# Optimization experiments

Hardware: AMD Instinct MI355X
Metric: run time of the kernel (lower is better)

Reference implementation:

```python
import jax, jax.numpy as jnp
import numpy as np

N = 50000
E = 800000
IN_DIM = 16
H = 128
L = 4
EDGE_DIM = 7
LN_EPS = 1e-5


def _linear_params(key, fan_in, fan_out):
    kw, kb = jax.random.split(key)
    w = jax.random.normal(kw, (fan_in, fan_out), jnp.float32) * 0.02
    b = jax.random.normal(kb, (fan_out,), jnp.float32) * 0.02
    return w, b


def setup_inputs() -> dict:
    key = jax.random.key(0)
    ks = jax.random.split(key, 20)
    x = jax.random.normal(ks[0], (N, IN_DIM), jnp.float32)
    pos = jax.random.uniform(ks[1], (N, 3), jnp.float32) * 10.0
    row = jax.random.randint(ks[2], (E,), 0, N, jnp.int32)
    # guarantee no self-loops so distance > 0 (radius_graph uses loop=False)
    off = jax.random.randint(ks[3], (E,), 1, N, jnp.int32)
    col = (row + off) % N
    edge_index = jnp.stack([row, col], axis=0)

    W_in, b_in = _linear_params(ks[4], IN_DIM, H)

    def stack_layers(kbase, fan_in, fan_out):
        ws, bs = [], []
        for l in range(L):
            w, b = _linear_params(jax.random.fold_in(kbase, l), fan_in, fan_out)
            ws.append(w); bs.append(b)
        return jnp.stack(ws), jnp.stack(bs)

    We1, be1 = stack_layers(ks[5], 2 * H + EDGE_DIM, H)
    We2, be2 = stack_layers(ks[6], H, H)
    We3, be3 = stack_layers(ks[7], H, H)
    Wn1, bn1 = stack_layers(ks[8], H + H, H)
    Wn2, bn2 = stack_layers(ks[9], H, H)
    Wn3, bn3 = stack_layers(ks[10], H, H)
    ln_g = jnp.ones((L, H), jnp.float32)
    ln_b = jnp.zeros((L, H), jnp.float32)

    return {
        'x': x, 'pos': pos, 'edge_index': edge_index,
        'W_in': W_in, 'b_in': b_in,
        'We1': We1, 'be1': be1, 'We2': We2, 'be2': be2, 'We3': We3, 'be3': be3,
        'Wn1': Wn1, 'bn1': bn1, 'Wn2': Wn2, 'bn2': bn2, 'Wn3': Wn3, 'bn3': bn3,
        'ln_g': ln_g, 'ln_b': ln_b,
    }


def reference(x, pos, edge_index, W_in, b_in, We1, be1, We2, be2, We3, be3,
              Wn1, bn1, Wn2, bn2, Wn3, bn3, ln_g, ln_b):
    n = x.shape[0]
    row, col = edge_index[0], edge_index[1]  # row=source, col=target (PyG)
    rel_pos = pos[col] - pos[row]                       # (E, 3)
    dist = jnp.linalg.norm(rel_pos, axis=1, keepdims=True)  # (E, 1)
    edge_attr = jnp.concatenate([rel_pos, dist], axis=1)    # (E, 4)

    h = x @ W_in + b_in  # (N, H)
    num_layers = We1.shape[0]
    for l in range(num_layers):
        mom = h[:, 3:6]
        rel_mom = mom[col] - mom[row]                        # (E, 3)
        ea = jnp.concatenate([edge_attr, rel_mom], axis=1)   # (E, 7)
        # PyG: x_i = x[target=col], x_j = x[source=row]; EdgeMLP concats [h_i, h_j, ea]
        m = jnp.concatenate([h[col], h[row], ea], axis=1)    # (E, 2H+7)
        m = jax.nn.relu(m @ We1[l] + be1[l])
        m = jax.nn.relu(m @ We2[l] + be2[l])
        m = m @ We3[l] + be3[l]                              # (E, H)
        agg = jax.ops.segment_sum(m, col, num_segments=n)    # scatter-add to targets
        u = jnp.concatenate([h, agg], axis=1)                # (N, 2H)
        u = jax.nn.relu(u @ Wn1[l] + bn1[l])
        u = jax.nn.relu(u @ Wn2[l] + bn2[l])
        u = u @ Wn3[l] + bn3[l]                              # (N, H)
        h = h + u
        mean = jnp.mean(h, axis=-1, keepdims=True)
        var = jnp.mean(jnp.square(h - mean), axis=-1, keepdims=True)
        h = (h - mean) * jax.lax.rsqrt(var + LN_EPS) * ln_g[l] + ln_b[l]
    return h
```

## Files before the change

kernel.cpp:

```cpp
#include <hip/hip_runtime.h>
#include <stdint.h>

#define NN 50000
#define NE 800000
#define HD 128
#define NL 4
#define NM 64
#define EB 128

typedef __bf16 bf16x8 __attribute__((ext_vector_type(8)));
typedef __bf16 bf16x4 __attribute__((ext_vector_type(4)));
typedef float  f32x4  __attribute__((ext_vector_type(4)));

__device__ __forceinline__ f32x4 mfma16(bf16x8 a, bf16x8 b, f32x4 c) {
  return __builtin_amdgcn_mfma_f32_16x16x32_bf16(a, b, c, 0, 0, 0);
}

template<int MT, int NT>
__device__ __forceinline__ void zero_acc(f32x4 (&acc)[MT][NT]) {
#pragma unroll
  for (int i = 0; i < MT; ++i)
#pragma unroll
    for (int j = 0; j < NT; ++j) acc[i][j] = f32x4{0.f, 0.f, 0.f, 0.f};
}

template<int MT, int NT, int KS>
__device__ __forceinline__ void gemm_chunk(const __bf16* A, int sa,
    const __bf16* __restrict__ Bt, int Krow, int k0,
    int m_off, int n_off, int lane, f32x4 (&acc)[MT][NT])
{
  const int arow = lane & 15;
  const int quad = lane >> 4;
  bf16x8 b[KS][NT];
#pragma unroll
  for (int ks = 0; ks < KS; ++ks)
#pragma unroll
    for (int nt = 0; nt < NT; ++nt)
      b[ks][nt] = *reinterpret_cast<const bf16x8*>(
          Bt + (size_t)(n_off + nt * 16 + arow) * Krow + k0 + ks * 32 + quad * 8);
#pragma unroll
  for (int ks = 0; ks < KS; ++ks) {
    const int k = k0 + ks * 32 + quad * 8;
    bf16x8 a[MT];
#pragma unroll
    for (int mt = 0; mt < MT; ++mt)
      a[mt] = *reinterpret_cast<const bf16x8*>(A + (m_off + mt * 16 + arow) * sa + k);
#pragma unroll
    for (int mt = 0; mt < MT; ++mt)
#pragma unroll
      for (int nt = 0; nt < NT; ++nt)
        acc[mt][nt] = mfma16(a[mt], b[ks][nt], acc[mt][nt]);
  }
}

template<int MT, int NT, bool RELU>
__device__ __forceinline__ void store_tile(__bf16* O, int so,
    const float* __restrict__ bias, int m_off, int n_off, int lane,
    f32x4 (&acc)[MT][NT])
{
  const int quad = lane >> 4;
  const int cl = lane & 15;
#pragma unroll
  for (int nt = 0; nt < NT; ++nt) {
    const int col = n_off + nt * 16 + cl;
    const float bv = bias[col];
#pragma unroll
    for (int mt = 0; mt < MT; ++mt)
#pragma unroll
      for (int r = 0; r < 4; ++r) {
        const int row = m_off + mt * 16 + quad * 4 + r;
        float v = acc[mt][nt][r] + bv;
        if (RELU) v = fmaxf(v, 0.f);
        O[row * so + col] = (__bf16)v;
      }
  }
}

__global__ void prep_w(const float* __restrict__ W, __bf16* __restrict__ Wt,
                       int K0, int Kp) {
  int idx = blockIdx.x * 256 + threadIdx.x;
  int total = NL * HD * Kp;
  if (idx >= total) return;
  int l = idx / (HD * Kp);
  int rem = idx - l * HD * Kp;
  int n = rem / Kp;
  int k = rem - n * Kp;
  float v = (k < K0) ? W[((size_t)l * K0 + k) * HD + n] : 0.f;
  Wt[idx] = (__bf16)v;
}

__global__ void prep_pqw(const float* __restrict__ We1,
                         __bf16* __restrict__ Wtopt, __bf16* __restrict__ Wbott) {
  int idx = blockIdx.x * 256 + threadIdx.x;
  if (idx >= NL * HD * HD) return;
  int l = idx / (HD * HD);
  int rem = idx - l * HD * HD;
  int n = rem >> 7;
  int k = rem & 127;
  const float* W = We1 + (size_t)l * 263 * HD;
  float extra = (k >= 3 && k < 6) ? W[(260 + k - 3) * HD + n] : 0.f;
  Wtopt[idx] = (__bf16)(W[k * HD + n] + extra);
  Wbott[idx] = (__bf16)(W[(128 + k) * HD + n] - extra);
}

__global__ void h0_kernel(const float* __restrict__ x, const float* __restrict__ W,
                          const float* __restrict__ b, float* __restrict__ H32,
                          __bf16* __restrict__ HB) {
  int idx = blockIdx.x * 256 + threadIdx.x;
  if (idx >= NN * HD) return;
  int node = idx >> 7, j = idx & 127;
  const float* xr = x + node * 16;
  float s = b[j];
#pragma unroll
  for (int k = 0; k < 16; ++k) s += xr[k] * W[k * HD + j];
  H32[idx] = s;
  HB[idx] = (__bf16)s;
}

__global__ void hist_kernel(const int* __restrict__ ei, int* __restrict__ cnt) {
  int e = blockIdx.x * 256 + threadIdx.x;
  if (e < NE) atomicAdd(&cnt[ei[NE + e]], 1);
}

__global__ void scan_kernel(const int* __restrict__ cnt, int* __restrict__ cur) {
  __shared__ int wsum[16];
  __shared__ int carry;
  int t = threadIdx.x;
  int lane = t & 63, wid = t >> 6;
  if (t == 0) carry = 0;
  __syncthreads();
  for (int base = 0; base < NN; base += 1024) {
    int v = (base + t < NN) ? cnt[base + t] : 0;
    int incl = v;
#pragma unroll
    for (int off = 1; off < 64; off <<= 1) {
      int u = __shfl_up(incl, off, 64);
      if (lane >= off) incl += u;
    }
    if (lane == 63) wsum[wid] = incl;
    __syncthreads();
    int woff = 0;
    for (int k = 0; k < wid; ++k) woff += wsum[k];
    int c = carry;
    if (base + t < NN) cur[base + t] = c + woff + incl - v;
    __syncthreads();
    if (t == 1023) carry = c + woff + incl;
    __syncthreads();
  }
}

__global__ void scatter_kernel(const int* __restrict__ ei, int* __restrict__ cur,
                               int* __restrict__ ROWS, int* __restrict__ COLS) {
  int e = blockIdx.x * 256 + threadIdx.x;
  if (e < NE) {
    int r = ei[e], c = ei[NE + e];
    int p = atomicAdd(&cur[c], 1);
    ROWS[p] = r;
    COLS[p] = c;
  }
}

__global__ void dist_kernel(const float* __restrict__ pos,
                            const int* __restrict__ ROWS, const int* __restrict__ COLS,
                            __bf16* __restrict__ DSTb) {
  int p = blockIdx.x * 256 + threadIdx.x;
  if (p >= NE) return;
  int r = ROWS[p], c = COLS[p];
  float dx = pos[c * 3 + 0] - pos[r * 3 + 0];
  float dy = pos[c * 3 + 1] - pos[r * 3 + 1];
  float dz = pos[c * 3 + 2] - pos[r * 3 + 2];
  DSTb[p] = (__bf16)sqrtf(dx * dx + dy * dy + dz * dz);
}

__global__ __launch_bounds__(256, 4) void pq_kernel(
    const __bf16* __restrict__ HB, const float* __restrict__ pos,
    const __bf16* __restrict__ Wtopt, const __bf16* __restrict__ Wbott,
    const float* __restrict__ W4xyz,
    const float* __restrict__ be1,
    __bf16* __restrict__ PB, __bf16* __restrict__ QB)
{
  const int task = blockIdx.x * 4 + (threadIdx.x >> 6);
  const int lane = threadIdx.x & 63;
  const int g = task & 1;
  const int base = (task >> 1) * 32;
  if (base >= NN) return;
  const int arow = lane & 15, quad = lane >> 4, cl = lane & 15;

  const __bf16* Wt = g ? Wbott : Wtopt;
  __bf16* O = g ? QB : PB;
  f32x4 acc[2][8];
  zero_acc(acc);
#pragma unroll
  for (int ks = 0; ks < 4; ++ks) {
    const int k = ks * 32 + quad * 8;
    bf16x8 b[8];
#pragma unroll
    for (int nt = 0; nt < 8; ++nt)
      b[nt] = *reinterpret_cast<const bf16x8*>(Wt + (size_t)(nt * 16 + arow) * HD + k);
    bf16x8 a[2];
#pragma unroll
    for (int mt = 0; mt < 2; ++mt) {
      int row = base + mt * 16 + arow;
      if (row >= NN) row = NN - 1;
      a[mt] = *reinterpret_cast<const bf16x8*>(HB + (size_t)row * HD + k);
    }
#pragma unroll
    for (int mt = 0; mt < 2; ++mt)
#pragma unroll
      for (int nt = 0; nt < 8; ++nt)
        acc[mt][nt] = mfma16(a[mt], b[nt], acc[mt][nt]);
  }
  float px[2][4], py[2][4], pz[2][4];
#pragma unroll
  for (int mt = 0; mt < 2; ++mt)
#pragma unroll
    for (int r = 0; r < 4; ++r) {
      int row = base + mt * 16 + quad * 4 + r;
      if (row >= NN) row = NN - 1;
      px[mt][r] = pos[row * 3 + 0];
      py[mt][r] = pos[row * 3 + 1];
      pz[mt][r] = pos[row * 3 + 2];
    }
#pragma unroll
  for (int nt = 0; nt < 8; ++nt) {
    const int col = nt * 16 + cl;
    const float w0 = W4xyz[col], w1 = W4xyz[HD + col], w2 = W4xyz[2 * HD + col];
    const float bb = g ? 0.f : be1[col];
#pragma unroll
    for (int mt = 0; mt < 2; ++mt)
#pragma unroll
      for (int r = 0; r < 4; ++r) {
        const int row = base + mt * 16 + quad * 4 + r;
        if (row < NN) {
          float dot = px[mt][r] * w0 + py[mt][r] * w1 + pz[mt][r] * w2;
          float v = acc[mt][nt][r] + (g ? -dot : dot) + bb;
          O[(size_t)row * HD + col] = (__bf16)v;
        }
      }
  }
}

__global__ __launch_bounds__(512, 4) void edge_kernel(
    const __bf16* __restrict__ PB, const __bf16* __restrict__ QB,
    const __bf16* __restrict__ DSTb,
    const int* __restrict__ ROWS, const int* __restrict__ COLS,
    const float* __restrict__ w4d,
    const __bf16* __restrict__ We2t, const __bf16* __restrict__ We3t,
    const float* __restrict__ be2, const float* __restrict__ be3,
    float* __restrict__ AGG)
{
  __shared__ __bf16 S1[EB * 136];
  __shared__ __bf16 S2[EB * 136];
  __shared__ float w4ds[HD], be2s[HD], be3s[HD];
  __shared__ int colS[EB];
  __shared__ unsigned long long bmaskS[EB / 64];
  const int t = threadIdx.x;

  const int nwg = gridDim.x;
  const int q = nwg >> 3, r8 = nwg & 7;
  const int xcd = blockIdx.x & 7, idx8 = blockIdx.x >> 3;
  const int bswz = (xcd < r8 ? xcd * (q + 1) : r8 * (q + 1) + (xcd - r8) * q) + idx8;
  const int base = bswz * EB;

  if (t < HD) { w4ds[t] = w4d[t]; be2s[t] = be2[t]; be3s[t] = be3[t]; }
  if (t < EB) colS[t] = COLS[base + t];
  __syncthreads();

  if (t < EB) {
    int d = (t == EB - 1) || (colS[t + 1] != colS[t]);
    unsigned long long bm = __ballot(d);
    if ((t & 63) == 0) bmaskS[t >> 6] = bm;
  }

  {
    const int i = t >> 2, cg = t & 3;
    const int p = base + i;
    const int c = colS[i];
    const int r = ROWS[p];
    const float dist = (float)DSTb[p];
    const __bf16* Prow = PB + (size_t)c * HD;
    const __bf16* Qrow = QB + (size_t)r * HD;
#pragma unroll
    for (int u = 0; u < 4; ++u) {
      const int ch = cg * 4 + u;
      bf16x8 pv = *reinterpret_cast<const bf16x8*>(Prow + ch * 8);
      bf16x8 qv = *reinterpret_cast<const bf16x8*>(Qrow + ch * 8);
      bf16x8 o;
#pragma unroll
      for (int j = 0; j < 8; ++j) {
        const int col = ch * 8 + j;
        float f = (float)pv[j] + (float)qv[j] + dist * w4ds[col];
        o[j] = (__bf16)fmaxf(f, 0.f);
      }
      *reinterpret_cast<bf16x8*>(S1 + i * 136 + ch * 8) = o;
    }
  }
  __syncthreads();

  const int w = t >> 6, lane = t & 63;
  const int m_off = (w >> 2) * 64, n_off = (w & 3) * 32;
  const int arow = lane & 15, quad = lane >> 4, cl = lane & 15;

  f32x4 acc[4][2];
#pragma unroll
  for (int g = 0; g < 2; ++g) {
    const __bf16* Wt = g ? We3t : We2t;
    const float* bs = g ? be3s : be2s;
    const __bf16* Sin  = g ? S2 : S1;
    __bf16* Sout = g ? S1 : S2;

    bf16x8 b[4][2];
#pragma unroll
    for (int ks = 0; ks < 4; ++ks)
#pragma unroll
      for (int nt = 0; nt < 2; ++nt)
        b[ks][nt] = *reinterpret_cast<const bf16x8*>(
            Wt + (size_t)(n_off + nt * 16 + arow) * HD + ks * 32 + quad * 8);

    zero_acc(acc);
#pragma unroll
    for (int ks = 0; ks < 4; ++ks) {
      const int k = ks * 32 + quad * 8;
      bf16x8 a[4];
#pragma unroll
      for (int mt = 0; mt < 4; ++mt)
        a[mt] = *reinterpret_cast<const bf16x8*>(Sin + (m_off + mt * 16 + arow) * 136 + k);
#pragma unroll
      for (int mt = 0; mt < 4; ++mt)
#pragma unroll
        for (int nt = 0; nt < 2; ++nt)
          acc[mt][nt] = mfma16(a[mt], b[ks][nt], acc[mt][nt]);
    }
#pragma unroll
    for (int nt = 0; nt < 2; ++nt) {
      const int col = n_off + nt * 16 + cl;
      const float bv = bs[col];
#pragma unroll
      for (int mt = 0; mt < 4; ++mt)
#pragma unroll
        for (int r = 0; r < 4; ++r) {
          const int row = m_off + mt * 16 + quad * 4 + r;
          float v = acc[mt][nt][r] + bv;
          if (!g) v = fmaxf(v, 0.f);
          Sout[row * 136 + col] = (__bf16)v;
        }
    }
    __syncthreads();
  }

  {
    const int j = t & 127, qtr = t >> 7;
    const int i0 = qtr * 32;
    unsigned int m = (unsigned int)(bmaskS[qtr >> 1] >> ((qtr & 1) * 32));
    m |= 0x80000000u;
    float s = 0.f;
    for (int r = 0; r < 32; ++r) {
      const int i = i0 + r;
      s += (float)S1[i * 136 + j];
      if ((m >> r) & 1u) {
        atomicAdd(&AGG[(size_t)colS[i] * HD + j], s);
        s = 0.f;
      }
    }
  }
}

__global__ __launch_bounds__(256, 4) void node_kernel(
    const __bf16* __restrict__ HBin, float* __restrict__ AGG,
    const __bf16* __restrict__ Wn1t, const __bf16* __restrict__ Wn2t,
    const __bf16* __restrict__ Wn3t,
    const float* __restrict__ bn1, const float* __restrict__ bn2,
    const float* __restrict__ bn3,
    const float* __restrict__ lng, const float* __restrict__ lnb,
    float* __restrict__ H32, __bf16* __restrict__ HBout,
    float* __restrict__ dout)
{
  __shared__ float SB[NM * 136];
  __shared__ float ps[NM][2], psq[NM][2];
  __shared__ float mean_s[NM], rstd_s[NM];
  __bf16* B16 = reinterpret_cast<__bf16*>(SB);
  const int t = threadIdx.x;
  const int base = blockIdx.x * NM;

  {
    const int i0 = t >> 4, s = t & 15;
#pragma unroll
    for (int g = 0; g < NM / 16; ++g) {
      const int i = g * 16 + i0;
      const int node = base + i;
      uint4 v = make_uint4(0, 0, 0, 0);
      if (node < NN) v = *(reinterpret_cast<const uint4*>(HBin + (size_t)node * HD) + s);
      *reinterpret_cast<uint4*>(&B16[i * 264 + s * 8]) = v;
    }
  }
  for (int idx = t; idx < NM * 32; idx += 256) {
    const int i = idx >> 5, c4 = idx & 31;
    const int node = base + i;
    float4 v = make_float4(0.f, 0.f, 0.f, 0.f);
    if (node < NN) {
      float4* ap = reinterpret_cast<float4*>(AGG + (size_t)node * HD + c4 * 4);
      v = *ap;
      *ap = make_float4(0.f, 0.f, 0.f, 0.f);
    }
    __bf16* d = &B16[i * 264 + HD + c4 * 4];
    d[0] = (__bf16)v.x; d[1] = (__bf16)v.y; d[2] = (__bf16)v.z; d[3] = (__bf16)v.w;
  }
  __syncthreads();

  const int w = t >> 6, lane = t & 63;
  const int m_off = (w >> 1) * 32, n_off = (w & 1) * 64;
  f32x4 acc[2][4];
  __bf16* reg0 = B16;
  __bf16* reg1 = B16 + NM * 136;

  zero_acc(acc);
  gemm_chunk<2, 4, 4>(B16, 264, Wn1t, 256, 0,   m_off, n_off, lane, acc);
  gemm_chunk<2, 4, 4>(B16, 264, Wn1t, 256, 128, m_off, n_off, lane, acc);
  __syncthreads();
  store_tile<2, 4, true>(reg0, 136, bn1, m_off, n_off, lane, acc);
  __syncthreads();
  zero_acc(acc);
  gemm_chunk<2, 4, 4>(reg0, 136, Wn2t, 128, 0, m_off, n_off, lane, acc);
  store_tile<2, 4, true>(reg1, 136, bn2, m_off, n_off, lane, acc);
  __syncthreads();
  zero_acc(acc);
  gemm_chunk<2, 4, 4>(reg1, 136, Wn3t, 128, 0, m_off, n_off, lane, acc);
  __syncthreads();

  {
    const int quad = lane >> 4, cl = lane & 15;
#pragma unroll
    for (int nt = 0; nt < 4; ++nt) {
      const int col = n_off + nt * 16 + cl;
      const float bv = bn3[col];
#pragma unroll
      for (int mt = 0; mt < 2; ++mt)
#pragma unroll
        for (int r = 0; r < 4; ++r) {
          const int row = m_off + mt * 16 + quad * 4 + r;
          const int node = base + row;
          float hv = (node < NN) ? H32[(size_t)node * HD + col] : 0.f;
          SB[row * 136 + col] = hv + acc[mt][nt][r] + bv;
        }
    }
  }
  __syncthreads();
  if (t < 128) {
    const int r = t >> 1, hh = t & 1;
    float s = 0.f, sq = 0.f;
    for (int j = hh * 64; j < hh * 64 + 64; ++j) {
      float v = SB[r * 136 + j];
      s += v; sq += v * v;
    }
    ps[r][hh] = s; psq[r][hh] = sq;
  }
  __syncthreads();
  if (t < NM) {
    float s = ps[t][0] + ps[t][1];
    float sq = psq[t][0] + psq[t][1];
    float mean = s * (1.f / HD);
    float var = sq * (1.f / HD) - mean * mean;
    mean_s[t] = mean;
    rstd_s[t] = rsqrtf(var + 1e-5f);
  }
  __syncthreads();
  for (int idx = t; idx < NM * HD; idx += 256) {
    const int r = idx >> 7, j = idx & 127;
    const int node = base + r;
    if (node < NN) {
      float v = (SB[r * 136 + j] - mean_s[r]) * rstd_s[r] * lng[j] + lnb[j];
      H32[(size_t)node * HD + j] = v;
      HBout[(size_t)node * HD + j] = (__bf16)v;
      if (dout) dout[(size_t)node * HD + j] = v;
    }
  }
}

extern "C" void kernel_launch(void* const* d_in, const int* in_sizes, int n_in,
                              void* d_out, int out_size, void* d_ws, size_t ws_size,
                              hipStream_t stream)
{
  const float* x    = (const float*)d_in[0];
  const float* pos  = (const float*)d_in[1];
  const int*   ei   = (const int*)d_in[2];
  const float* W_in = (const float*)d_in[3];
  const float* b_in = (const float*)d_in[4];
  const float* We1  = (const float*)d_in[5];
  const float* be1  = (const float*)d_in[6];
  const float* We2  = (const float*)d_in[7];
  const float* be2  = (const float*)d_in[8];
  const float* We3  = (const float*)d_in[9];
  const float* be3  = (const float*)d_in[10];
  const float* Wn1  = (const float*)d_in[11];
  const float* bn1  = (const float*)d_in[12];
  const float* Wn2  = (const float*)d_in[13];
  const float* bn2  = (const float*)d_in[14];
  const float* Wn3  = (const float*)d_in[15];
  const float* bn3  = (const float*)d_in[16];
  const float* lng  = (const float*)d_in[17];
  const float* lnb  = (const float*)d_in[18];
  float* out = (float*)d_out;

  char* ws = (char*)d_ws;
  size_t off = 0;
  auto alloc = [&](size_t bytes) -> char* {
    char* p = ws + off;
    off += (bytes + 255) & ~(size_t)255;
    return p;
  };
  __bf16* Wtopt = (__bf16*)alloc((size_t)NL * HD * HD * 2);
  __bf16* Wbott = (__bf16*)alloc((size_t)NL * HD * HD * 2);
  __bf16* We2t = (__bf16*)alloc((size_t)NL * HD * HD * 2);
  __bf16* We3t = (__bf16*)alloc((size_t)NL * HD * HD * 2);
  __bf16* Wn1t = (__bf16*)alloc((size_t)NL * HD * 256 * 2);
  __bf16* Wn2t = (__bf16*)alloc((size_t)NL * HD * HD * 2);
  __bf16* Wn3t = (__bf16*)alloc((size_t)NL * HD * HD * 2);
  __bf16* DSTb = (__bf16*)alloc((size_t)NE * 2);
  float*  H32  = (float*) alloc((size_t)NN * HD * 4);
  __bf16* HB   = (__bf16*)alloc((size_t)NN * HD * 2);
  __bf16* PB   = (__bf16*)alloc((size_t)NN * HD * 2);
  __bf16* QB   = (__bf16*)alloc((size_t)NN * HD * 2);
  float*  AGG  = (float*) alloc((size_t)NN * HD * 4);
  int*    CNT  = (int*)   alloc((size_t)NN * 4);
  int*    CUR  = (int*)   alloc((size_t)NN * 4);
  int*    ROWS = (int*)   alloc((size_t)NE * 4);
  int*    COLS = (int*)   alloc((size_t)NE * 4);

  hipMemsetAsync(CNT, 0, (size_t)NN * 4, stream);
  hipMemsetAsync(AGG, 0, (size_t)NN * HD * 4, stream);
  prep_pqw<<<(NL * HD * HD + 255) / 256, 256, 0, stream>>>(We1, Wtopt, Wbott);
  prep_w<<<(NL * HD * HD + 255) / 256, 256, 0, stream>>>(We2, We2t, 128, 128);
  prep_w<<<(NL * HD * HD + 255) / 256, 256, 0, stream>>>(We3, We3t, 128, 128);
  prep_w<<<(NL * HD * 256 + 255) / 256, 256, 0, stream>>>(Wn1, Wn1t, 256, 256);
  prep_w<<<(NL * HD * HD + 255) / 256, 256, 0, stream>>>(Wn2, Wn2t, 128, 128);
  prep_w<<<(NL * HD * HD + 255) / 256, 256, 0, stream>>>(Wn3, Wn3t, 128, 128);
  h0_kernel<<<(NN * HD + 255) / 256, 256, 0, stream>>>(x, W_in, b_in, H32, HB);
  hist_kernel<<<(NE + 255) / 256, 256, 0, stream>>>(ei, CNT);
  scan_kernel<<<1, 1024, 0, stream>>>(CNT, CUR);
  scatter_kernel<<<(NE + 255) / 256, 256, 0, stream>>>(ei, CUR, ROWS, COLS);
  dist_kernel<<<(NE + 255) / 256, 256, 0, stream>>>(pos, ROWS, COLS, DSTb);

  const int pq_tasks = 2 * ((NN + 31) / 32);
  const int pq_blocks = (pq_tasks + 3) / 4;
  for (int l = 0; l < NL; ++l) {
    const float* We1l = We1 + (size_t)l * 263 * HD;
    pq_kernel<<<pq_blocks, 256, 0, stream>>>(HB, pos,
        Wtopt + (size_t)l * HD * HD, Wbott + (size_t)l * HD * HD,
        We1l + 256 * HD,
        be1 + l * HD, PB, QB);
    edge_kernel<<<NE / EB, 512, 0, stream>>>(PB, QB, DSTb, ROWS, COLS,
        We1l + 259 * HD,
        We2t + (size_t)l * HD * HD, We3t + (size_t)l * HD * HD,
        be2 + l * HD, be3 + l * HD, AGG);
    node_kernel<<<(NN + NM - 1) / NM, 256, 0, stream>>>(HB, AGG,
        Wn1t + (size_t)l * HD * 256, Wn2t + (size_t)l * HD * HD,
        Wn3t + (size_t)l * HD * HD,
        bn1 + l * HD, bn2 + l * HD, bn3 + l * HD,
        lng + l * HD, lnb + l * HD,
        H32, HB, (l == NL - 1) ? out : nullptr);
  }
}
```

Before: 1.242 ms.

## Process two edge tiles per block with software-pipelined gather prefetch

The edge kernel now handles two 128-edge tiles per workgroup. While the MLP of the current tile runs, it prefetches the next tile's row/col indices, distances and Q rows into registers, then builds the next tile's first-layer activations into the free shared buffer while the current tile's scatter-add runs. The grid is halved. This hides gather latency and amortizes the weight and bias setup, at the cost of higher register pressure, fewer blocks in flight and serialized tiles within a block.

```diff
diff --git a/kernel.cpp b/kernel.cpp
--- a/kernel.cpp
+++ b/kernel.cpp
@@ -7,6 +7,7 @@
 #define NL 4
 #define NM 64
 #define EB 128
+#define TPB 2
 
 typedef __bf16 bf16x8 __attribute__((ext_vector_type(8)));
 typedef __bf16 bf16x4 __attribute__((ext_vector_type(4)));
@@ -249,50 +250,51 @@
     const float* __restrict__ be2, const float* __restrict__ be3,
     float* __restrict__ AGG)
 {
-  __shared__ __bf16 S1[EB * 136];
-  __shared__ __bf16 S2[EB * 136];
+  __shared__ __bf16 SA[EB * 136];
+  __shared__ __bf16 SBuf[EB * 136];
   __shared__ float w4ds[HD], be2s[HD], be3s[HD];
-  __shared__ int colS[EB];
-  __shared__ unsigned long long bmaskS[EB / 64];
+  __shared__ int colS[2][EB];
+  __shared__ unsigned long long bmaskS[2][2];
   const int t = threadIdx.x;
 
   const int nwg = gridDim.x;
   const int q = nwg >> 3, r8 = nwg & 7;
   const int xcd = blockIdx.x & 7, idx8 = blockIdx.x >> 3;
   const int bswz = (xcd < r8 ? xcd * (q + 1) : r8 * (q + 1) + (xcd - r8) * q) + idx8;
-  const int base = bswz * EB;
+  const int base0 = bswz * (EB * TPB);
+
+  const int i = t >> 2, cg = t & 3;
 
   if (t < HD) { w4ds[t] = w4d[t]; be2s[t] = be2[t]; be3s[t] = be3[t]; }
-  if (t < EB) colS[t] = COLS[base + t];
-  __syncthreads();
-
-  if (t < EB) {
-    int d = (t == EB - 1) || (colS[t + 1] != colS[t]);
-    unsigned long long bm = __ballot(d);
-    if ((t & 63) == 0) bmaskS[t >> 6] = bm;
-  }
-
+  if (t < EB) colS[0][t] = COLS[base0 + t];
   {
-    const int i = t >> 2, cg = t & 3;
-    const int p = base + i;
-    const int c = colS[i];
-    const int r = ROWS[p];
-    const float dist = (float)DSTb[p];
-    const __bf16* Prow = PB + (size_t)c * HD;
-    const __bf16* Qrow = QB + (size_t)r * HD;
+    const int p0 = base0 + i;
+    const int r0 = ROWS[p0];
+    const int c0 = COLS[p0];
+    const float dist0 = (float)DSTb[p0];
+    bf16x8 qv[4];
+#pragma unroll
+    for (int u = 0; u < 4; ++u)
+      qv[u] = *reinterpret_cast<const bf16x8*>(QB + (size_t)r0 * HD + (cg * 4 + u) * 8);
+    __syncthreads();
+    if (t < EB) {
+      int d = (t == EB - 1) || (colS[0][t + 1] != colS[0][t]);
+      unsigned long long bm = __ballot(d);
+      if ((t & 63) == 0) bmaskS[0][t >> 6] = bm;
+    }
+    const __bf16* Prow = PB + (size_t)c0 * HD;
 #pragma unroll
     for (int u = 0; u < 4; ++u) {
       const int ch = cg * 4 + u;
       bf16x8 pv = *reinterpret_cast<const bf16x8*>(Prow + ch * 8);
-      bf16x8 qv = *reinterpret_cast<const bf16x8*>(Qrow + ch * 8);
       bf16x8 o;
 #pragma unroll
       for (int j = 0; j < 8; ++j) {
         const int col = ch * 8 + j;
-        float f = (float)pv[j] + (float)qv[j] + dist * w4ds[col];
+        float f = (float)pv[j] + (float)qv[u][j] + dist0 * w4ds[col];
         o[j] = (__bf16)fmaxf(f, 0.f);
       }
-      *reinterpret_cast<bf16x8*>(S1 + i * 136 + ch * 8) = o;
+      *reinterpret_cast<bf16x8*>(SA + i * 136 + ch * 8) = o;
     }
   }
   __syncthreads();
@@ -301,67 +303,113 @@
   const int m_off = (w >> 2) * 64, n_off = (w & 3) * 32;
   const int arow = lane & 15, quad = lane >> 4, cl = lane & 15;
 
+  __bf16* X = SA;
+  __bf16* Y = SBuf;
   f32x4 acc[4][2];
-#pragma unroll
-  for (int g = 0; g < 2; ++g) {
-    const __bf16* Wt = g ? We3t : We2t;
-    const float* bs = g ? be3s : be2s;
-    const __bf16* Sin  = g ? S2 : S1;
-    __bf16* Sout = g ? S1 : S2;
-
-    bf16x8 b[4][2];
-#pragma unroll
-    for (int ks = 0; ks < 4; ++ks)
-#pragma unroll
-      for (int nt = 0; nt < 2; ++nt)
-        b[ks][nt] = *reinterpret_cast<const bf16x8*>(
-            Wt + (size_t)(n_off + nt * 16 + arow) * HD + ks * 32 + quad * 8);
-
-    zero_acc(acc);
-#pragma unroll
-    for (int ks = 0; ks < 4; ++ks) {
-      const int k = ks * 32 + quad * 8;
-      bf16x8 a[4];
-#pragma unroll
-      for (int mt = 0; mt < 4; ++mt)
-        a[mt] = *reinterpret_cast<const bf16x8*>(Sin + (m_off + mt * 16 + arow) * 136 + k);
-#pragma unroll
-      for (int mt = 0; mt < 4; ++mt)
+  bf16x8 qv[4];
+  int c_nxt = 0; float dist_nxt = 0.f;
+
+#pragma unroll
+  for (int tt = 0; tt < TPB; ++tt) {
+    if (tt + 1 < TPB) {
+      const int tb = base0 + (tt + 1) * EB;
+      if (t < EB) colS[(tt + 1) & 1][t] = COLS[tb + t];
+      const int pn = tb + i;
+      const int r_nxt = ROWS[pn];
+      c_nxt = COLS[pn];
+      dist_nxt = (float)DSTb[pn];
+#pragma unroll
+      for (int u = 0; u < 4; ++u)
+        qv[u] = *reinterpret_cast<const bf16x8*>(QB + (size_t)r_nxt * HD + (cg * 4 + u) * 8);
+    }
+
+#pragma unroll
+    for (int g = 0; g < 2; ++g) {
+      const __bf16* Wt = g ? We3t : We2t;
+      const float* bs = g ? be3s : be2s;
+      const __bf16* Sin = g ? Y : X;
+      __bf16* Sout = g ? X : Y;
+
+      bf16x8 b[4][2];
+#pragma unroll
+      for (int ks = 0; ks < 4; ++ks)
 #pragma unroll
         for (int nt = 0; nt < 2; ++nt)
-          acc[mt][nt] = mfma16(a[mt], b[ks][nt], acc[mt][nt]);
-    }
-#pragma unroll
-    for (int nt = 0; nt < 2; ++nt) {
-      const int col = n_off + nt * 16 + cl;
-      const float bv = bs[col];
-#pragma unroll
-      for (int mt = 0; mt < 4; ++mt)
-#pragma unroll
-        for (int r = 0; r < 4; ++r) {
-          const int row = m_off + mt * 16 + quad * 4 + r;
-          float v = acc[mt][nt][r] + bv;
-          if (!g) v = fmaxf(v, 0.f);
-          Sout[row * 136 + col] = (__bf16)v;
+          b[ks][nt] = *reinterpret_cast<const bf16x8*>(
+              Wt + (size_t)(n_off + nt * 16 + arow) * HD + ks * 32 + quad * 8);
+
+      zero_acc(acc);
+#pragma unroll
+      for (int ks = 0; ks < 4; ++ks) {
+        const int k = ks * 32 + quad * 8;
+        bf16x8 a[4];
+#pragma unroll
+        for (int mt = 0; mt < 4; ++mt)
+          a[mt] = *reinterpret_cast<const bf16x8*>(Sin + (m_off + mt * 16 + arow) * 136 + k);
+#pragma unroll
+        for (int mt = 0; mt < 4; ++mt)
+#pragma unroll
+          for (int nt = 0; nt < 2; ++nt)
+            acc[mt][nt] = mfma16(a[mt], b[ks][nt], acc[mt][nt]);
+      }
+#pragma unroll
+      for (int nt = 0; nt < 2; ++nt) {
+        const int col = n_off + nt * 16 + cl;
+        const float bv = bs[col];
+#pragma unroll
+        for (int mt = 0; mt < 4; ++mt)
+#pragma unroll
+          for (int r = 0; r < 4; ++r) {
+            const int row = m_off + mt * 16 + quad * 4 + r;
+            float v = acc[mt][nt][r] + bv;
+            if (!g) v = fmaxf(v, 0.f);
+            Sout[row * 136 + col] = (__bf16)v;
+          }
+      }
+      __syncthreads();
+    }
+
+    if (tt + 1 < TPB) {
+      const int par = (tt + 1) & 1;
+      if (t < EB) {
+        int d = (t == EB - 1) || (colS[par][t + 1] != colS[par][t]);
+        unsigned long long bm = __ballot(d);
+        if ((t & 63) == 0) bmaskS[par][t >> 6] = bm;
+      }
+      const __bf16* Prow = PB + (size_t)c_nxt * HD;
+#pragma unroll
+      for (int u = 0; u < 4; ++u) {
+        const int ch = cg * 4 + u;
+        bf16x8 pv = *reinterpret_cast<const bf16x8*>(Prow + ch * 8);
+        bf16x8 o;
+#pragma unroll
+        for (int j = 0; j < 8; ++j) {
+          const int col = ch * 8 + j;
+          float f = (float)pv[j] + (float)qv[u][j] + dist_nxt * w4ds[col];
+          o[j] = (__bf16)fmaxf(f, 0.f);
         }
+        *reinterpret_cast<bf16x8*>(Y + i * 136 + ch * 8) = o;
+      }
+    }
+
+    {
+      const int par = tt & 1;
+      const int j = t & 127, qtr = t >> 7;
+      const int i0 = qtr * 32;
+      unsigned int m = (unsigned int)(bmaskS[par][qtr >> 1] >> ((qtr & 1) * 32));
+      m |= 0x80000000u;
+      float s = 0.f;
+      for (int r = 0; r < 32; ++r) {
+        const int ii = i0 + r;
+        s += (float)X[ii * 136 + j];
+        if ((m >> r) & 1u) {
+          atomicAdd(&AGG[(size_t)colS[par][ii] * HD + j], s);
+          s = 0.f;
+        }
+      }
     }
     __syncthreads();
-  }
-
-  {
-    const int j = t & 127, qtr = t >> 7;
-    const int i0 = qtr * 32;
-    unsigned int m = (unsigned int)(bmaskS[qtr >> 1] >> ((qtr & 1) * 32));
-    m |= 0x80000000u;
-    float s = 0.f;
-    for (int r = 0; r < 32; ++r) {
-      const int i = i0 + r;
-      s += (float)S1[i * 136 + j];
-      if ((m >> r) & 1u) {
-        atomicAdd(&AGG[(size_t)colS[i] * HD + j], s);
-        s = 0.f;
-      }
-    }
+    __bf16* tmp = X; X = Y; Y = tmp;
   }
 }
 
@@ -548,7 +596,7 @@
         Wtopt + (size_t)l * HD * HD, Wbott + (size_t)l * HD * HD,
         We1l + 256 * HD,
         be1 + l * HD, PB, QB);
-    edge_kernel<<<NE / EB, 512, 0, stream>>>(PB, QB, DSTb, ROWS, COLS,
+    edge_kernel<<<NE / (EB * TPB), 512, 0, stream>>>(PB, QB, DSTb, ROWS, COLS,
         We1l + 259 * HD,
         We2t + (size_t)l * HD * HD, We3t + (size_t)l * HD * HD,
         be2 + l * HD, be3 + l * HD, AGG);
```

New measurement: 1.258 ms. No clear change (+1.2%).
